# Optimization experiments

Measured on AMD Instinct MI355X. Metric: run time of the kernel, lower is better.

## Reference

```python
import jax, jax.numpy as jnp
import numpy as np

N_NODES = 50000
N_EDGES = 800000
IN_CH = 128
HID = 64
OUT_CH = 64


def sage_conv(x, src, dst, w_l, w_r, b, num_nodes):
    """PyG SAGEConv with mean aggregation: lin_l(mean_j x_j) + lin_r(x_i)."""
    # gather source features and scatter-mean into destination nodes
    agg = jax.ops.segment_sum(x[src], dst, num_segments=num_nodes)          # [N, C]
    deg = jax.ops.segment_sum(jnp.ones((src.shape[0],), x.dtype), dst,
                              num_segments=num_nodes)                        # [N]
    mean = agg / jnp.maximum(deg, 1.0)[:, None]
    return mean @ w_l + x @ w_r + b


def setup_inputs() -> dict:
    key = jax.random.key(0)
    k = jax.random.split(key, 8)
    x = jax.random.normal(k[0], (N_NODES, IN_CH), dtype=jnp.float32)
    edge_index = jax.random.randint(k[1], (2, N_EDGES), 0, N_NODES, dtype=jnp.int32)
    s1 = 1.0 / np.sqrt(IN_CH)
    s2 = 1.0 / np.sqrt(HID)
    w1_l = jax.random.uniform(k[2], (IN_CH, HID), jnp.float32, -s1, s1)
    w1_r = jax.random.uniform(k[3], (IN_CH, HID), jnp.float32, -s1, s1)
    b1 = jax.random.uniform(k[4], (HID,), jnp.float32, -s1, s1)
    w2_l = jax.random.uniform(k[5], (HID, OUT_CH), jnp.float32, -s2, s2)
    w2_r = jax.random.uniform(k[6], (HID, OUT_CH), jnp.float32, -s2, s2)
    b2 = jax.random.uniform(k[7], (OUT_CH,), jnp.float32, -s2, s2)
    return {"x": x, "edge_index": edge_index,
            "w1_l": w1_l, "w1_r": w1_r, "b1": b1,
            "w2_l": w2_l, "w2_r": w2_r, "b2": b2}


def reference(x, edge_index, w1_l, w1_r, b1, w2_l, w2_r, b2):
    src, dst = edge_index[0], edge_index[1]
    num_nodes = x.shape[0]
    h = jax.nn.relu(sage_conv(x, src, dst, w1_l, w1_r, b1, num_nodes))
    out = jax.nn.relu(sage_conv(h, src, dst, w2_l, w2_r, b2, num_nodes))
    return out
```

## Files before the change

### kernel.cpp

```cpp
#include <hip/hip_runtime.h>
#include <hip/hip_fp16.h>

#define DEGCAP 64
#define TILE 4000

typedef _Float16 half8 __attribute__((ext_vector_type(8)));
typedef _Float16 half4v __attribute__((ext_vector_type(4)));
typedef float float4v __attribute__((ext_vector_type(4)));

__global__ __launch_bounds__(256) void fused_scatter_gemm1(
        const int* __restrict__ src, const int* __restrict__ dst,
        int* __restrict__ gCursor, unsigned short* __restrict__ ssrc,
        int E, int scatterBlocks,
        const float* __restrict__ A, const float* __restrict__ Wl,
        const float* __restrict__ Wr, unsigned short* __restrict__ Clh,
        unsigned short* __restrict__ Trh, int M) {
    constexpr int K = 128, KP = K + 8;
    __shared__ __align__(16) char smem[(64 + 128) * KP * 2];

    const int tid = threadIdx.x;

    if ((int)blockIdx.x < scatterBlocks) {
        const int t0 = blockIdx.x * TILE;
        const int len = (E - t0) < TILE ? (E - t0) : TILE;
        for (int j = tid; j < len; j += 256) {
            int d = dst[t0 + j];
            int s = src[t0 + j];
            int pos = atomicAdd(&gCursor[d], 1);
            if (pos < DEGCAP)
                ssrc[(long long)d * DEGCAP + pos] = (unsigned short)s;
        }
    } else {
        _Float16* xs  = (_Float16*)smem;
        _Float16* wsh = (_Float16*)(smem + 64 * KP * 2);

        const int row0 = ((int)blockIdx.x - scatterBlocks) * 64;

        for (int i = tid; i < 128 * (K / 4); i += 256) {
            int c = i & 127, kv = i >> 7;
            const float* W = (c < 64) ? Wl : Wr;
            int cc = c & 63;
            half4v hv;
            hv.x = (_Float16)W[(kv * 4 + 0) * 64 + cc];
            hv.y = (_Float16)W[(kv * 4 + 1) * 64 + cc];
            hv.z = (_Float16)W[(kv * 4 + 2) * 64 + cc];
            hv.w = (_Float16)W[(kv * 4 + 3) * 64 + cc];
            *(half4v*)&wsh[c * KP + kv * 4] = hv;
        }
        for (int i = tid; i < 64 * (K / 4); i += 256) {
            int r = i & 63, kv = i >> 6;
            int gr = row0 + r;
            float4 v = make_float4(0.f, 0.f, 0.f, 0.f);
            if (gr < M) v = *(const float4*)&A[(long long)gr * K + kv * 4];
            half4v hv;
            hv.x = (_Float16)v.x; hv.y = (_Float16)v.y;
            hv.z = (_Float16)v.z; hv.w = (_Float16)v.w;
            *(half4v*)&xs[r * KP + kv * 4] = hv;
        }
        __syncthreads();

        const int wv = tid >> 6;
        const int lane = tid & 63;
        const int qd = lane >> 4;
        const int lr = lane & 15;

        float4v accL[4], accR[4];
        #pragma unroll
        for (int i = 0; i < 4; ++i) {
            accL[i] = (float4v){0.f, 0.f, 0.f, 0.f};
            accR[i] = (float4v){0.f, 0.f, 0.f, 0.f};
        }

        #pragma unroll
        for (int s = 0; s < K / 32; ++s) {
            const int k0 = s * 32 + qd * 8;
            half8 bl = *(half8*)&wsh[(wv * 16 + lr) * KP + k0];
            half8 br = *(half8*)&wsh[(64 + wv * 16 + lr) * KP + k0];
            #pragma unroll
            for (int i = 0; i < 4; ++i) {
                half8 a = *(half8*)&xs[(i * 16 + lr) * KP + k0];
                accL[i] = __builtin_amdgcn_mfma_f32_16x16x32_f16(a, bl, accL[i], 0, 0, 0);
                accR[i] = __builtin_amdgcn_mfma_f32_16x16x32_f16(a, br, accR[i], 0, 0, 0);
            }
        }

        const int col = wv * 16 + lr;
        #pragma unroll
        for (int i = 0; i < 4; ++i) {
            #pragma unroll
            for (int rg = 0; rg < 4; ++rg) {
                int gr = row0 + i * 16 + qd * 4 + rg;
                if (gr < M) {
                    Clh[(long long)gr * 64 + col] = __half_as_ushort(__float2half_rn(accL[i][rg]));
                    Trh[(long long)gr * 64 + col] = __half_as_ushort(__float2half_rn(accR[i][rg]));
                }
            }
        }
    }
}

template <int K>
__global__ __launch_bounds__(256) void gemm_mfma_h(const unsigned short* __restrict__ Ah,
                                                   const float* __restrict__ Wl,
                                                   const float* __restrict__ Wr,
                                                   unsigned short* __restrict__ Clh,
                                                   unsigned short* __restrict__ Trh,
                                                   int M) {
    constexpr int KP = K + 8;
    __shared__ _Float16 xs[64 * KP];
    __shared__ _Float16 wsh[128 * KP];

    const int tid = threadIdx.x;
    const int row0 = blockIdx.x * 64;

    for (int i = tid; i < 128 * (K / 4); i += 256) {
        int c = i & 127, kv = i >> 7;
        const float* W = (c < 64) ? Wl : Wr;
        int cc = c & 63;
        half4v hv;
        hv.x = (_Float16)W[(kv * 4 + 0) * 64 + cc];
        hv.y = (_Float16)W[(kv * 4 + 1) * 64 + cc];
        hv.z = (_Float16)W[(kv * 4 + 2) * 64 + cc];
        hv.w = (_Float16)W[(kv * 4 + 3) * 64 + cc];
        *(half4v*)&wsh[c * KP + kv * 4] = hv;
    }
    for (int i = tid; i < 64 * (K / 4); i += 256) {
        int r = i & 63, kv = i >> 6;
        int gr = row0 + r;
        ushort4 u = make_ushort4(0, 0, 0, 0);
        if (gr < M) u = *(const ushort4*)&Ah[(long long)gr * K + kv * 4];
        *(ushort4*)&xs[r * KP + kv * 4] = u;
    }
    __syncthreads();

    const int wv = tid >> 6;
    const int lane = tid & 63;
    const int qd = lane >> 4;
    const int lr = lane & 15;

    float4v accL[4], accR[4];
    #pragma unroll
    for (int i = 0; i < 4; ++i) {
        accL[i] = (float4v){0.f, 0.f, 0.f, 0.f};
        accR[i] = (float4v){0.f, 0.f, 0.f, 0.f};
    }

    #pragma unroll
    for (int s = 0; s < K / 32; ++s) {
        const int k0 = s * 32 + qd * 8;
        half8 bl = *(half8*)&wsh[(wv * 16 + lr) * KP + k0];
        half8 br = *(half8*)&wsh[(64 + wv * 16 + lr) * KP + k0];
        #pragma unroll
        for (int i = 0; i < 4; ++i) {
            half8 a = *(half8*)&xs[(i * 16 + lr) * KP + k0];
            accL[i] = __builtin_amdgcn_mfma_f32_16x16x32_f16(a, bl, accL[i], 0, 0, 0);
            accR[i] = __builtin_amdgcn_mfma_f32_16x16x32_f16(a, br, accR[i], 0, 0, 0);
        }
    }

    const int col = wv * 16 + lr;
    #pragma unroll
    for (int i = 0; i < 4; ++i) {
        #pragma unroll
        for (int rg = 0; rg < 4; ++rg) {
            int gr = row0 + i * 16 + qd * 4 + rg;
            if (gr < M) {
                Clh[(long long)gr * 64 + col] = __half_as_ushort(__float2half_rn(accL[i][rg]));
                Trh[(long long)gr * 64 + col] = __half_as_ushort(__float2half_rn(accR[i][rg]));
            }
        }
    }
}

template <bool OUTH>
__global__ __launch_bounds__(256) void agg_combine(const unsigned int* __restrict__ tl2,
                                                   const unsigned int* __restrict__ trh2,
                                                   const float* __restrict__ bias,
                                                   const int* __restrict__ cnt,
                                                   const unsigned short* __restrict__ ssrc,
                                                   void* __restrict__ outv, int N) {
    int w = (blockIdx.x * 256 + threadIdx.x) >> 6;
    int lane = threadIdx.x & 63;
    if (w >= N) return;
    int deg = cnt[w];
    int n = deg < DEGCAP ? deg : DEGCAP;
    int c2 = lane & 31;
    int half = lane >> 5;

    int sid = (lane < n) ? (int)ssrc[(long long)w * DEGCAP + lane] : 0;

    float x0 = 0.f, y0 = 0.f, x1 = 0.f, y1 = 0.f;
    float x2 = 0.f, y2 = 0.f, x3 = 0.f, y3 = 0.f;
    float x4 = 0.f, y4 = 0.f, x5 = 0.f, y5 = 0.f;
    float x6 = 0.f, y6 = 0.f, x7 = 0.f, y7 = 0.f;

    int jj = 0;
    for (; jj + 16 <= n; jj += 16) {
        int e0 = __shfl(sid, jj + 0 + half, 64);
        int e1 = __shfl(sid, jj + 2 + half, 64);
        int e2 = __shfl(sid, jj + 4 + half, 64);
        int e3 = __shfl(sid, jj + 6 + half, 64);
        int e4 = __shfl(sid, jj + 8 + half, 64);
        int e5 = __shfl(sid, jj + 10 + half, 64);
        int e6 = __shfl(sid, jj + 12 + half, 64);
        int e7 = __shfl(sid, jj + 14 + half, 64);
        unsigned int u0 = tl2[e0 * 32 + c2];
        unsigned int u1 = tl2[e1 * 32 + c2];
        unsigned int u2 = tl2[e2 * 32 + c2];
        unsigned int u3 = tl2[e3 * 32 + c2];
        unsigned int u4 = tl2[e4 * 32 + c2];
        unsigned int u5 = tl2[e5 * 32 + c2];
        unsigned int u6 = tl2[e6 * 32 + c2];
        unsigned int u7 = tl2[e7 * 32 + c2];
        float2 f0 = __half22float2(*(__half2*)&u0);
        float2 f1 = __half22float2(*(__half2*)&u1);
        float2 f2 = __half22float2(*(__half2*)&u2);
        float2 f3 = __half22float2(*(__half2*)&u3);
        float2 f4 = __half22float2(*(__half2*)&u4);
        float2 f5 = __half22float2(*(__half2*)&u5);
        float2 f6 = __half22float2(*(__half2*)&u6);
        float2 f7 = __half22float2(*(__half2*)&u7);
        x0 += f0.x; y0 += f0.y;  x1 += f1.x; y1 += f1.y;
        x2 += f2.x; y2 += f2.y;  x3 += f3.x; y3 += f3.y;
        x4 += f4.x; y4 += f4.y;  x5 += f5.x; y5 += f5.y;
        x6 += f6.x; y6 += f6.y;  x7 += f7.x; y7 += f7.y;
    }
    for (; jj + 8 <= n; jj += 8) {
        int e0 = __shfl(sid, jj + 0 + half, 64);
        int e1 = __shfl(sid, jj + 2 + half, 64);
        int e2 = __shfl(sid, jj + 4 + half, 64);
        int e3 = __shfl(sid, jj + 6 + half, 64);
        unsigned int u0 = tl2[e0 * 32 + c2];
        unsigned int u1 = tl2[e1 * 32 + c2];
        unsigned int u2 = tl2[e2 * 32 + c2];
        unsigned int u3 = tl2[e3 * 32 + c2];
        float2 f0 = __half22float2(*(__half2*)&u0);
        float2 f1 = __half22float2(*(__half2*)&u1);
        float2 f2 = __half22float2(*(__half2*)&u2);
        float2 f3 = __half22float2(*(__half2*)&u3);
        x0 += f0.x; y0 += f0.y;  x1 += f1.x; y1 += f1.y;
        x2 += f2.x; y2 += f2.y;  x3 += f3.x; y3 += f3.y;
    }
    for (; jj < n; jj += 2) {
        int e = __shfl(sid, jj + half, 64);
        if (jj + half < n) {
            unsigned int u = tl2[e * 32 + c2];
            float2 f = __half22float2(*(__half2*)&u);
            x0 += f.x; y0 += f.y;
        }
    }

    float sx = ((x0 + x1) + (x2 + x3)) + ((x4 + x5) + (x6 + x7));
    float sy = ((y0 + y1) + (y2 + y3)) + ((y4 + y5) + (y6 + y7));
    sx += __shfl_xor(sx, 32, 64);
    sy += __shfl_xor(sy, 32, 64);
    if (half == 0) {
        int c = c2 * 2;
        float d = (float)(deg > 1 ? deg : 1);
        unsigned int tu = trh2[(long long)w * 32 + c2];
        float2 t = __half22float2(*(__half2*)&tu);
        float2 bb = *(const float2*)&bias[c];
        float v0 = fmaxf(sx / d + t.x + bb.x, 0.f);
        float v1 = fmaxf(sy / d + t.y + bb.y, 0.f);
        if (OUTH) {
            __half2 hv = __floats2half2_rn(v0, v1);
            ((unsigned int*)outv)[(long long)w * 32 + c2] = *(unsigned int*)&hv;
        } else {
            ((float2*)outv)[(long long)w * 32 + c2] = make_float2(v0, v1);
        }
    }
}

extern "C" void kernel_launch(void* const* d_in, const int* in_sizes, int n_in,
                              void* d_out, int out_size, void* d_ws, size_t ws_size,
                              hipStream_t stream) {
    const float* x   = (const float*)d_in[0];
    const int*   ei  = (const int*)d_in[1];
    const float* w1l = (const float*)d_in[2];
    const float* w1r = (const float*)d_in[3];
    const float* b1  = (const float*)d_in[4];
    const float* w2l = (const float*)d_in[5];
    const float* w2r = (const float*)d_in[6];
    const float* b2  = (const float*)d_in[7];
    float* out = (float*)d_out;

    const int N = in_sizes[0] / 128;
    const int E = in_sizes[1] / 2;
    const int* src = ei;
    const int* dst = ei + E;

    auto alignup = [](size_t v) { return (v + 255) & ~(size_t)255; };
    char* p = (char*)d_ws;
    int* gCursor = (int*)p;                   p += alignup((size_t)N * sizeof(int));
    unsigned short* ssrc = (unsigned short*)p; p += alignup((size_t)N * DEGCAP * sizeof(unsigned short));
    const long long NC = (long long)N * 64;
    unsigned short* tlh = (unsigned short*)p; p += alignup((size_t)NC * sizeof(unsigned short));
    unsigned short* trh = (unsigned short*)p; p += alignup((size_t)NC * sizeof(unsigned short));
    unsigned short* hh  = (unsigned short*)p; p += alignup((size_t)NC * sizeof(unsigned short));

    const int scatterBlocks = (E + TILE - 1) / TILE;
    const int gemmBlocks = (N + 63) / 64;
    const int aggBlocks = (int)((NC + 255) / 256);

    hipMemsetAsync(gCursor, 0, (size_t)N * sizeof(int), stream);

    fused_scatter_gemm1<<<scatterBlocks + gemmBlocks, 256, 0, stream>>>(
        src, dst, gCursor, ssrc, E, scatterBlocks,
        x, w1l, w1r, tlh, trh, N);

    agg_combine<true><<<aggBlocks, 256, 0, stream>>>((const unsigned int*)tlh,
                                                     (const unsigned int*)trh,
                                                     b1, gCursor, ssrc, hh, N);

    gemm_mfma_h<64><<<gemmBlocks, 256, 0, stream>>>(hh, w2l, w2r, tlh, trh, N);
    agg_combine<false><<<aggBlocks, 256, 0, stream>>>((const unsigned int*)tlh,
                                                      (const unsigned int*)trh,
                                                      b2, gCursor, ssrc, out, N);
}
```

Baseline: 184.6 us.

## Pre-transpose fp16 weights once and feed MFMA GEMMs directly from global memory

A new prep kernel zeroes the degree cursor (replacing the memset) and converts both layers' weight matrices into transposed fp16 buffers. Both GEMM kernels drop their LDS staging and __syncthreads. Each wave now loads its weight fragments from the transposed buffer into registers and reads A rows straight from global memory into MFMA operands. This removes per-block strided fp32 weight conversion and LDS round trips, at the cost of one extra kernel launch and less coalesced per-lane global reads for A.

New measurement: 189.3 us. 2.6% more time.

```diff
diff --git a/kernel.cpp b/kernel.cpp
--- a/kernel.cpp
+++ b/kernel.cpp
@@ -5,19 +5,39 @@
 #define TILE 4000
 
 typedef _Float16 half8 __attribute__((ext_vector_type(8)));
-typedef _Float16 half4v __attribute__((ext_vector_type(4)));
 typedef float float4v __attribute__((ext_vector_type(4)));
+
+__global__ __launch_bounds__(256) void prep(int* __restrict__ gCursor,
+                                            const float* __restrict__ w1l,
+                                            const float* __restrict__ w1r,
+                                            const float* __restrict__ w2l,
+                                            const float* __restrict__ w2r,
+                                            _Float16* __restrict__ Wt1,
+                                            _Float16* __restrict__ Wt2, int N) {
+    int idx = blockIdx.x * 256 + threadIdx.x;
+    if (idx < N) { gCursor[idx] = 0; return; }
+    int j = idx - N;
+    if (j < 128 * 128) {
+        int c = j >> 7, k = j & 127;
+        const float* W = (c < 64) ? w1l : w1r;
+        Wt1[c * 128 + k] = (_Float16)W[k * 64 + (c & 63)];
+        return;
+    }
+    j -= 128 * 128;
+    if (j < 128 * 64) {
+        int c = j >> 6, k = j & 63;
+        const float* W = (c < 64) ? w2l : w2r;
+        Wt2[c * 64 + k] = (_Float16)W[k * 64 + (c & 63)];
+    }
+}
 
 __global__ __launch_bounds__(256) void fused_scatter_gemm1(
         const int* __restrict__ src, const int* __restrict__ dst,
         int* __restrict__ gCursor, unsigned short* __restrict__ ssrc,
         int E, int scatterBlocks,
-        const float* __restrict__ A, const float* __restrict__ Wl,
-        const float* __restrict__ Wr, unsigned short* __restrict__ Clh,
-        unsigned short* __restrict__ Trh, int M) {
-    constexpr int K = 128, KP = K + 8;
-    __shared__ __align__(16) char smem[(64 + 128) * KP * 2];
-
+        const float* __restrict__ A, const _Float16* __restrict__ Wt1,
+        unsigned short* __restrict__ Clh, unsigned short* __restrict__ Trh,
+        int M) {
     const int tid = threadIdx.x;
 
     if ((int)blockIdx.x < scatterBlocks) {
@@ -31,39 +51,20 @@
                 ssrc[(long long)d * DEGCAP + pos] = (unsigned short)s;
         }
     } else {
-        _Float16* xs  = (_Float16*)smem;
-        _Float16* wsh = (_Float16*)(smem + 64 * KP * 2);
-
         const int row0 = ((int)blockIdx.x - scatterBlocks) * 64;
-
-        for (int i = tid; i < 128 * (K / 4); i += 256) {
-            int c = i & 127, kv = i >> 7;
-            const float* W = (c < 64) ? Wl : Wr;
-            int cc = c & 63;
-            half4v hv;
-            hv.x = (_Float16)W[(kv * 4 + 0) * 64 + cc];
-            hv.y = (_Float16)W[(kv * 4 + 1) * 64 + cc];
-            hv.z = (_Float16)W[(kv * 4 + 2) * 64 + cc];
-            hv.w = (_Float16)W[(kv * 4 + 3) * 64 + cc];
-            *(half4v*)&wsh[c * KP + kv * 4] = hv;
-        }
-        for (int i = tid; i < 64 * (K / 4); i += 256) {
-            int r = i & 63, kv = i >> 6;
-            int gr = row0 + r;
-            float4 v = make_float4(0.f, 0.f, 0.f, 0.f);
-            if (gr < M) v = *(const float4*)&A[(long long)gr * K + kv * 4];
-            half4v hv;
-            hv.x = (_Float16)v.x; hv.y = (_Float16)v.y;
-            hv.z = (_Float16)v.z; hv.w = (_Float16)v.w;
-            *(half4v*)&xs[r * KP + kv * 4] = hv;
-        }
-        __syncthreads();
-
         const int wv = tid >> 6;
         const int lane = tid & 63;
         const int qd = lane >> 4;
         const int lr = lane & 15;
 
+        half8 bl[4], br[4];
+        const int colL = wv * 16 + lr;
+        #pragma unroll
+        for (int s = 0; s < 4; ++s) {
+            bl[s] = *(const half8*)&Wt1[colL * 128 + s * 32 + qd * 8];
+            br[s] = *(const half8*)&Wt1[(64 + colL) * 128 + s * 32 + qd * 8];
+        }
+
         float4v accL[4], accR[4];
         #pragma unroll
         for (int i = 0; i < 4; ++i) {
@@ -72,15 +73,26 @@
         }
 
         #pragma unroll
-        for (int s = 0; s < K / 32; ++s) {
-            const int k0 = s * 32 + qd * 8;
-            half8 bl = *(half8*)&wsh[(wv * 16 + lr) * KP + k0];
-            half8 br = *(half8*)&wsh[(64 + wv * 16 + lr) * KP + k0];
+        for (int i = 0; i < 4; ++i) {
+            const int gr = row0 + i * 16 + lr;
+            const bool ok = gr < M;
+            const float* Arow = &A[(long long)gr * 128];
             #pragma unroll
-            for (int i = 0; i < 4; ++i) {
-                half8 a = *(half8*)&xs[(i * 16 + lr) * KP + k0];
-                accL[i] = __builtin_amdgcn_mfma_f32_16x16x32_f16(a, bl, accL[i], 0, 0, 0);
-                accR[i] = __builtin_amdgcn_mfma_f32_16x16x32_f16(a, br, accR[i], 0, 0, 0);
+            for (int s = 0; s < 4; ++s) {
+                const int k0 = s * 32 + qd * 8;
+                float4 a0 = make_float4(0.f, 0.f, 0.f, 0.f);
+                float4 a1 = make_float4(0.f, 0.f, 0.f, 0.f);
+                if (ok) {
+                    a0 = *(const float4*)&Arow[k0];
+                    a1 = *(const float4*)&Arow[k0 + 4];
+                }
+                half8 a;
+                a[0] = (_Float16)a0.x; a[1] = (_Float16)a0.y;
+                a[2] = (_Float16)a0.z; a[3] = (_Float16)a0.w;
+                a[4] = (_Float16)a1.x; a[5] = (_Float16)a1.y;
+                a[6] = (_Float16)a1.z; a[7] = (_Float16)a1.w;
+                accL[i] = __builtin_amdgcn_mfma_f32_16x16x32_f16(a, bl[s], accL[i], 0, 0, 0);
+                accR[i] = __builtin_amdgcn_mfma_f32_16x16x32_f16(a, br[s], accR[i], 0, 0, 0);
             }
         }
 
@@ -99,44 +111,25 @@
     }
 }
 
-template <int K>
-__global__ __launch_bounds__(256) void gemm_mfma_h(const unsigned short* __restrict__ Ah,
-                                                   const float* __restrict__ Wl,
-                                                   const float* __restrict__ Wr,
+__global__ __launch_bounds__(256) void gemm2_nolds(const unsigned short* __restrict__ Ah,
+                                                   const _Float16* __restrict__ Wt2,
                                                    unsigned short* __restrict__ Clh,
                                                    unsigned short* __restrict__ Trh,
                                                    int M) {
-    constexpr int KP = K + 8;
-    __shared__ _Float16 xs[64 * KP];
-    __shared__ _Float16 wsh[128 * KP];
-
     const int tid = threadIdx.x;
     const int row0 = blockIdx.x * 64;
-
-    for (int i = tid; i < 128 * (K / 4); i += 256) {
-        int c = i & 127, kv = i >> 7;
-        const float* W = (c < 64) ? Wl : Wr;
-        int cc = c & 63;
-        half4v hv;
-        hv.x = (_Float16)W[(kv * 4 + 0) * 64 + cc];
-        hv.y = (_Float16)W[(kv * 4 + 1) * 64 + cc];
-        hv.z = (_Float16)W[(kv * 4 + 2) * 64 + cc];
-        hv.w = (_Float16)W[(kv * 4 + 3) * 64 + cc];
-        *(half4v*)&wsh[c * KP + kv * 4] = hv;
-    }
-    for (int i = tid; i < 64 * (K / 4); i += 256) {
-        int r = i & 63, kv = i >> 6;
-        int gr = row0 + r;
-        ushort4 u = make_ushort4(0, 0, 0, 0);
-        if (gr < M) u = *(const ushort4*)&Ah[(long long)gr * K + kv * 4];
-        *(ushort4*)&xs[r * KP + kv * 4] = u;
-    }
-    __syncthreads();
-
     const int wv = tid >> 6;
     const int lane = tid & 63;
     const int qd = lane >> 4;
     const int lr = lane & 15;
+
+    half8 bl[2], br[2];
+    const int colL = wv * 16 + lr;
+    #pragma unroll
+    for (int s = 0; s < 2; ++s) {
+        bl[s] = *(const half8*)&Wt2[colL * 64 + s * 32 + qd * 8];
+        br[s] = *(const half8*)&Wt2[(64 + colL) * 64 + s * 32 + qd * 8];
+    }
 
     float4v accL[4], accR[4];
     #pragma unroll
@@ -146,15 +139,16 @@
     }
 
     #pragma unroll
-    for (int s = 0; s < K / 32; ++s) {
-        const int k0 = s * 32 + qd * 8;
-        half8 bl = *(half8*)&wsh[(wv * 16 + lr) * KP + k0];
-        half8 br = *(half8*)&wsh[(64 + wv * 16 + lr) * KP + k0];
-        #pragma unroll
-        for (int i = 0; i < 4; ++i) {
-            half8 a = *(half8*)&xs[(i * 16 + lr) * KP + k0];
-            accL[i] = __builtin_amdgcn_mfma_f32_16x16x32_f16(a, bl, accL[i], 0, 0, 0);
-            accR[i] = __builtin_amdgcn_mfma_f32_16x16x32_f16(a, br, accR[i], 0, 0, 0);
+    for (int i = 0; i < 4; ++i) {
+        const int gr = row0 + i * 16 + lr;
+        const bool ok = gr < M;
+        const _Float16* Arow = (const _Float16*)&Ah[(long long)gr * 64];
+        #pragma unroll
+        for (int s = 0; s < 2; ++s) {
+            half8 a = (half8){0, 0, 0, 0, 0, 0, 0, 0};
+            if (ok) a = *(const half8*)&Arow[s * 32 + qd * 8];
+            accL[i] = __builtin_amdgcn_mfma_f32_16x16x32_f16(a, bl[s], accL[i], 0, 0, 0);
+            accR[i] = __builtin_amdgcn_mfma_f32_16x16x32_f16(a, br[s], accR[i], 0, 0, 0);
         }
     }
 
@@ -297,22 +291,26 @@
     unsigned short* tlh = (unsigned short*)p; p += alignup((size_t)NC * sizeof(unsigned short));
     unsigned short* trh = (unsigned short*)p; p += alignup((size_t)NC * sizeof(unsigned short));
     unsigned short* hh  = (unsigned short*)p; p += alignup((size_t)NC * sizeof(unsigned short));
+    _Float16* Wt1 = (_Float16*)p;             p += alignup(128 * 128 * sizeof(_Float16));
+    _Float16* Wt2 = (_Float16*)p;             p += alignup(128 * 64 * sizeof(_Float16));
 
     const int scatterBlocks = (E + TILE - 1) / TILE;
     const int gemmBlocks = (N + 63) / 64;
     const int aggBlocks = (int)((NC + 255) / 256);
 
-    hipMemsetAsync(gCursor, 0, (size_t)N * sizeof(int), stream);
+    const int prepWork = N + 128 * 128 + 128 * 64;
+    prep<<<(prepWork + 255) / 256, 256, 0, stream>>>(gCursor, w1l, w1r, w2l, w2r,
+                                                     Wt1, Wt2, N);
 
     fused_scatter_gemm1<<<scatterBlocks + gemmBlocks, 256, 0, stream>>>(
         src, dst, gCursor, ssrc, E, scatterBlocks,
-        x, w1l, w1r, tlh, trh, N);
+        x, Wt1, tlh, trh, N);
 
     agg_combine<true><<<aggBlocks, 256, 0, stream>>>((const unsigned int*)tlh,
                                                      (const unsigned int*)trh,
                                                      b1, gCursor, ssrc, hh, N);
 
-    gemm_mfma_h<64><<<gemmBlocks, 256, 0, stream>>>(hh, w2l, w2r, tlh, trh, N);
+    gemm2_nolds<<<gemmBlocks, 256, 0, stream>>>(hh, Wt2, tlh, trh, N);
     agg_combine<false><<<aggBlocks, 256, 0, stream>>>((const unsigned int*)tlh,
                                                       (const unsigned int*)trh,
                                                       b2, gCursor, ssrc, out, N);
```
